# Kernel tuning notes

Hardware: AMD Instinct MI355X
Metric: run time of the kernel (lower is better)

## Reference

```python
import jax, jax.numpy as jnp
import numpy as np

B, C, H, W = 32, 512, 32, 32
R = C // 2  # reduced channels for key/prod projections


def setup_inputs() -> dict:
    key = jax.random.key(0)
    ks = jax.random.split(key, 8)
    s_in = 1.0 / np.sqrt(C)
    return {
        "x": jax.random.normal(ks[0], (B, C, H, W), jnp.float32),
        "Wk": jax.random.normal(ks[1], (R, C), jnp.float32) * s_in,
        "bk": jax.random.normal(ks[2], (R,), jnp.float32) * s_in,
        "Wp": jax.random.normal(ks[3], (R, C), jnp.float32) * s_in,
        "bp": jax.random.normal(ks[4], (R,), jnp.float32) * s_in,
        "Wv": jax.random.normal(ks[5], (C, C), jnp.float32) * s_in,
        "bv": jax.random.normal(ks[6], (C,), jnp.float32) * s_in,
        "param": jax.random.normal(ks[7], (1,), jnp.float32),
    }


def _conv1x1(x, Wmat, b):
    # 1x1 conv on NCHW == per-pixel channel matmul
    return jnp.einsum('bchw,oc->bohw', x, Wmat) + b[None, :, None, None]


def reference(x, Wk, bk, Wp, bp, Wv, bv, param):
    b, c, h, w = x.shape
    hw = h * w
    f_key = _conv1x1(x, Wk, bk).reshape(b, -1, hw).transpose(0, 2, 1)  # [B,HW,R]
    f_prod = _conv1x1(x, Wp, bp).reshape(b, -1, hw)                    # [B,R,HW]
    f_value = _conv1x1(x, Wv, bv).reshape(b, -1, hw)                   # [B,C,HW]
    energy = jnp.einsum('bnr,brm->bnm', f_key, f_prod)                 # [B,HW,HW]
    similarity = jax.nn.softmax(energy, axis=-1)
    # bmm(f_value, similarity^T): out[b,c,n] = sum_m f_value[b,c,m] * sim[b,n,m]
    attended = jnp.einsum('bcm,bnm->bcn', f_value, similarity).reshape(b, c, h, w)
    return x + attended * param
```

## Files before the change

### kernel.cpp

```cpp
#include <hip/hip_runtime.h>
#include <hip/hip_bf16.h>

#define BATCH 32
#define CCH   512
#define HWSZ  1024
#define RCH   256

typedef __attribute__((ext_vector_type(8))) _Float16 f16x8;
typedef __attribute__((ext_vector_type(4))) float f32x4;

__device__ __forceinline__ ushort f2h(float f) {
    _Float16 h = (_Float16)f;
    ushort u; __builtin_memcpy(&u, &h, 2);
    return u;
}
__device__ __forceinline__ float h2f(ushort u) {
    _Float16 h; __builtin_memcpy(&h, &u, 2);
    return (float)h;
}

__device__ __forceinline__ void load_lds16(const void* g, void* l) {
    __builtin_amdgcn_global_load_lds((const __attribute__((address_space(1))) void*)g,
                                     (__attribute__((address_space(3))) void*)l,
                                     16, 0, 0);
}

__device__ __forceinline__ void xcd_swizzle(int& bx, int& by, int& bz) {
    int gx = gridDim.x, gy = gridDim.y;
    int n   = gx * gy * gridDim.z;
    int lin = bx + gx * (by + gy * bz);
    int cpx = n >> 3;
    int s = (lin & 7) * cpx + (lin >> 3);
    bx = s % gx; s /= gx;
    by = s % gy;
    bz = s / gy;
}

__global__ __launch_bounds__(256) void k_pre(
    const float* __restrict__ x, ushort* __restrict__ xt,
    const float* __restrict__ Wk, const float* __restrict__ bk,
    const float* __restrict__ Wp, const float* __restrict__ bp,
    const float* __restrict__ Wv,
    ushort* __restrict__ Wkp_h, ushort* __restrict__ Wv_h, float* __restrict__ bias_kp)
{
    __shared__ float tile[64][68];
    int t = threadIdx.x;
    if (blockIdx.z == 32) {
        int base = ((blockIdx.y * 16 + blockIdx.x) * 256 + t) * 8;
        int o = base >> 9, c = base & 511;
        const float* srcKP = (o < 256) ? (Wk + (size_t)o * 512 + c)
                                       : (Wp + (size_t)(o - 256) * 512 + c);
        float4 a0 = *(const float4*)srcKP;
        float4 a1 = *(const float4*)(srcKP + 4);
        ushort4 h0, h1;
        h0.x = f2h(a0.x); h0.y = f2h(a0.y); h0.z = f2h(a0.z); h0.w = f2h(a0.w);
        h1.x = f2h(a1.x); h1.y = f2h(a1.y); h1.z = f2h(a1.z); h1.w = f2h(a1.w);
        *(ushort4*)&Wkp_h[base] = h0;
        *(ushort4*)&Wkp_h[base + 4] = h1;
        float4 v0 = *(const float4*)(Wv + base);
        float4 v1 = *(const float4*)(Wv + base + 4);
        h0.x = f2h(v0.x); h0.y = f2h(v0.y); h0.z = f2h(v0.z); h0.w = f2h(v0.w);
        h1.x = f2h(v1.x); h1.y = f2h(v1.y); h1.z = f2h(v1.z); h1.w = f2h(v1.w);
        *(ushort4*)&Wv_h[base] = h0;
        *(ushort4*)&Wv_h[base + 4] = h1;
        if (c == 0) bias_kp[o] = (o < 256) ? bk[o] : bp[o - 256];
        return;
    }
    int b  = blockIdx.z;
    int c0 = blockIdx.y * 64;
    int n0 = blockIdx.x * 64;
    const float* xb = x + (size_t)b * CCH * HWSZ;
    int tc  = t >> 4;
    int tn4 = (t & 15) * 4;
    #pragma unroll
    for (int i = 0; i < 4; ++i) {
        int c = tc + i * 16;
        *(float4*)&tile[c][tn4] = *(const float4*)&xb[(size_t)(c0 + c) * HWSZ + n0 + tn4];
    }
    __syncthreads();
    ushort* oh = xt + (size_t)b * HWSZ * CCH;
    int tn  = t >> 4;
    int tc4 = (t & 15) * 4;
    #pragma unroll
    for (int i = 0; i < 4; ++i) {
        int n = tn + i * 16;
        ushort4 h;
        h.x = f2h(tile[tc4 + 0][n]);
        h.y = f2h(tile[tc4 + 1][n]);
        h.z = f2h(tile[tc4 + 2][n]);
        h.w = f2h(tile[tc4 + 3][n]);
        *(ushort4*)&oh[(size_t)(n0 + n) * CCH + c0 + tc4] = h;
    }
}

template<int MODE>
__global__ __launch_bounds__(512, 4) void k_gemm8(
    const ushort* __restrict__ A, const ushort* __restrict__ B,
    int lda, int ldb, long aBatch, long bBatch,
    float* __restrict__ outF, ushort* __restrict__ out16,
    long oBatch, int ldo,
    const float* __restrict__ bias,
    const float* __restrict__ xres, const float* __restrict__ param,
    int NT)
{
    __shared__ ushort lds[2][12288];
    int bx = blockIdx.x, by = blockIdx.y, bz = blockIdx.z;
    xcd_swizzle(bx, by, bz);
    const int z  = bz;
    const int m0 = bx * 128;
    const int n0 = by * 256;
    const int t    = threadIdx.x;
    const int lane = t & 63;
    const int w    = t >> 6;
    const int wm = w >> 2, wn = w & 3;
    const int l15 = lane & 15;
    const int hi  = lane >> 4;
    const int G   = hi ^ ((lane >> 1) & 3);

    const ushort* Ab = A + (size_t)z * aBatch;
    const ushort* Bb = B + (size_t)z * bBatch;

    const int sr = t >> 2;
    const int sg = (t & 3) ^ ((t >> 3) & 3);

    f32x4 acc[4][4] = {};
    f16x8 a[4], b01[2], b23[2];

#define STAGE(slot, kt) do {                                                 \
        size_t sa_ = (size_t)(m0 + sr) * lda + (kt) * 32 + sg * 8;           \
        load_lds16(Ab + sa_, &lds[slot][t * 8]);                             \
        size_t sb_ = (size_t)(n0 + sr) * ldb + (kt) * 32 + sg * 8;           \
        load_lds16(Bb + sb_, &lds[slot][4096 + t * 8]);                      \
        load_lds16(Bb + sb_ + (size_t)128 * ldb, &lds[slot][8192 + t * 8]);  \
    } while (0)

#define RD_ALL(slot) do {                                                    \
        _Pragma("unroll")                                                    \
        for (int ni = 0; ni < 2; ++ni)                                       \
            b01[ni] = *(const f16x8*)&lds[slot][4096 + (wn * 64 + ni * 16 + l15) * 32 + G * 8]; \
        _Pragma("unroll")                                                    \
        for (int ni = 0; ni < 2; ++ni)                                       \
            b23[ni] = *(const f16x8*)&lds[slot][4096 + (wn * 64 + 32 + ni * 16 + l15) * 32 + G * 8]; \
        _Pragma("unroll")                                                    \
        for (int mi = 0; mi < 4; ++mi)                                       \
            a[mi] = *(const f16x8*)&lds[slot][(wm * 64 + mi * 16 + l15) * 32 + G * 8]; \
    } while (0)

#define BAR() __builtin_amdgcn_s_barrier()
#define WLG(N) do { asm volatile("s_waitcnt lgkmcnt(" #N ")" ::: "memory");  \
                    __builtin_amdgcn_sched_barrier(0); } while (0)
#define WVM(N) asm volatile("s_waitcnt vmcnt(" #N ")" ::: "memory")

#define MM4(mi) do {                                                         \
        acc[mi][0] = __builtin_amdgcn_mfma_f32_16x16x32_f16(a[mi], b01[0], acc[mi][0], 0, 0, 0); \
        acc[mi][1] = __builtin_amdgcn_mfma_f32_16x16x32_f16(a[mi], b01[1], acc[mi][1], 0, 0, 0); \
        acc[mi][2] = __builtin_amdgcn_mfma_f32_16x16x32_f16(a[mi], b23[0], acc[mi][2], 0, 0, 0); \
        acc[mi][3] = __builtin_amdgcn_mfma_f32_16x16x32_f16(a[mi], b23[1], acc[mi][3], 0, 0, 0); \
    } while (0)

#define MFMA_PIPE() do {                                                     \
        WLG(3); MM4(0); WLG(2); MM4(1); WLG(1); MM4(2); WLG(0); MM4(3);      \
    } while (0)

    STAGE(0, 0);
    WVM(0);
    BAR();

    for (int j = 0; j < NT - 1; ++j) {
        int cur = j & 1;
        STAGE(cur ^ 1, j + 1);
        RD_ALL(cur);
        MFMA_PIPE();
        WVM(0);
        BAR();
    }
    {
        RD_ALL(1);
        MFMA_PIPE();
    }

    if (MODE == 3) {
        float* fbuf = (float*)lds;
        const float prm = param[0];
        float*       ob = outF + (size_t)z * oBatch;
        const float* xb = xres + (size_t)z * oBatch;
        #pragma unroll
        for (int h = 0; h < 4; ++h) {
            asm volatile("s_waitcnt lgkmcnt(0)" ::: "memory");
            BAR();
            if (wn == h) {
                #pragma unroll
                for (int mi = 0; mi < 4; ++mi)
                    #pragma unroll
                    for (int ni = 0; ni < 4; ++ni) {
                        int cc = (ni >> 1) * 32 + (ni & 1) * 16 + l15;
                        int nn = (wm * 64 + mi * 16 + hi * 4) ^ ((cc & 7) << 2);
                        *(f32x4*)&fbuf[cc * 128 + nn] = acc[mi][ni];
                    }
            }
            asm volatile("s_waitcnt lgkmcnt(0)" ::: "memory");
            BAR();
            #pragma unroll
            for (int rr = 0; rr < 4; ++rr) {
                int cc  = w * 8 + rr * 2 + (lane >> 5);
                int col = (lane & 31) * 4;
                f32x4 o4 = *(const f32x4*)&fbuf[cc * 128 + (col ^ ((cc & 7) << 2))];
                size_t g = (size_t)(n0 + h * 64 + cc) * ldo + m0 + col;
                float4 xv = *(const float4*)&xb[g];
                float4 ov;
                ov.x = xv.x + o4[0] * prm;
                ov.y = xv.y + o4[1] * prm;
                ov.z = xv.z + o4[2] * prm;
                ov.w = xv.w + o4[3] * prm;
                *(float4*)&ob[g] = ov;
            }
        }
    } else {
        #pragma unroll
        for (int mi = 0; mi < 4; ++mi) {
            #pragma unroll
            for (int ni = 0; ni < 4; ++ni) {
                int gc  = n0 + wn * 64 + (ni >> 1) * 32 + (ni & 1) * 16 + l15;
                int gr0 = m0 + wm * 64 + mi * 16 + hi * 4;
                #pragma unroll
                for (int jj = 0; jj < 4; ++jj) {
                    int gr = gr0 + jj;
                    float v = acc[mi][ni][jj];
                    if (MODE == 0) {
                        v += bias[gc];
                        out16[(size_t)gr * ldo + gc] = f2h(v);
                    } else if (MODE == 1) {
                        v += bias[gr];
                        out16[(size_t)z * oBatch + (size_t)gr * ldo + gc] = f2h(v);
                    } else {
                        out16[(size_t)z * oBatch + (size_t)gr * ldo + gc] = f2h(v);
                    }
                }
            }
        }
    }
#undef STAGE
#undef RD_ALL
#undef BAR
#undef WLG
#undef WVM
#undef MM4
#undef MFMA_PIPE
}

__global__ __launch_bounds__(256) void k_softmax(ushort* __restrict__ E)
{
    int t    = threadIdx.x;
    int rowi = t >> 7;
    int tl   = t & 127;
    ushort* row = E + (size_t)(blockIdx.x * 2 + rowi) * HWSZ;
    uint4 u = *(const uint4*)&row[tl * 8];
    float v[8];
    v[0] = h2f(u.x & 0xffff); v[1] = h2f(u.x >> 16);
    v[2] = h2f(u.y & 0xffff); v[3] = h2f(u.y >> 16);
    v[4] = h2f(u.z & 0xffff); v[5] = h2f(u.z >> 16);
    v[6] = h2f(u.w & 0xffff); v[7] = h2f(u.w >> 16);
    float mx = v[0];
    #pragma unroll
    for (int i = 1; i < 8; ++i) mx = fmaxf(mx, v[i]);
    #pragma unroll
    for (int off = 1; off < 64; off <<= 1)
        mx = fmaxf(mx, __shfl_xor(mx, off));
    __shared__ float redm[2][2];
    __shared__ float reds[2][2];
    int lane = t & 63, wv = (t >> 6) & 1;
    if (lane == 0) redm[rowi][wv] = mx;
    __syncthreads();
    mx = fmaxf(redm[rowi][0], redm[rowi][1]);
    float s = 0.f;
    #pragma unroll
    for (int i = 0; i < 8; ++i) { v[i] = __expf(v[i] - mx); s += v[i]; }
    #pragma unroll
    for (int off = 1; off < 64; off <<= 1)
        s += __shfl_xor(s, off);
    if (lane == 0) reds[rowi][wv] = s;
    __syncthreads();
    s = reds[rowi][0] + reds[rowi][1];
    float inv = 1.0f / s;
    uint4 o;
    o.x = (unsigned)f2h(v[0] * inv) | ((unsigned)f2h(v[1] * inv) << 16);
    o.y = (unsigned)f2h(v[2] * inv) | ((unsigned)f2h(v[3] * inv) << 16);
    o.z = (unsigned)f2h(v[4] * inv) | ((unsigned)f2h(v[5] * inv) << 16);
    o.w = (unsigned)f2h(v[6] * inv) | ((unsigned)f2h(v[7] * inv) << 16);
    *(uint4*)&row[tl * 8] = o;
}

extern "C" void kernel_launch(void* const* d_in, const int* in_sizes, int n_in,
                              void* d_out, int out_size, void* d_ws, size_t ws_size,
                              hipStream_t stream)
{
    const float* x    = (const float*)d_in[0];
    const float* Wk   = (const float*)d_in[1];
    const float* bk   = (const float*)d_in[2];
    const float* Wp   = (const float*)d_in[3];
    const float* bp   = (const float*)d_in[4];
    const float* Wv   = (const float*)d_in[5];
    const float* bv   = (const float*)d_in[6];
    const float* prm  = (const float*)d_in[7];
    float* out = (float*)d_out;
    char* ws = (char*)d_ws;

    const size_t SZ16 = (size_t)BATCH * HWSZ * CCH * 2;
    ushort* xt    = (ushort*)(ws + 0);
    ushort* KPt   = (ushort*)(ws + SZ16);
    ushort* fv    = (ushort*)(ws + 2 * SZ16);
    ushort* E     = (ushort*)(ws + 3 * SZ16);
    char* wbase   = ws + 3 * SZ16 + (size_t)BATCH * HWSZ * HWSZ * 2;
    ushort* Wkp_h = (ushort*)(wbase);
    ushort* Wv_h  = (ushort*)(wbase + 524288);
    float*  bias_kp = (float*)(wbase + 2 * 524288);

    k_pre<<<dim3(16, 8, 33), 256, 0, stream>>>(
        x, xt, Wk, bk, Wp, bp, Wv, Wkp_h, Wv_h, bias_kp);

    k_gemm8<0><<<dim3(256, 2, 1), 512, 0, stream>>>(
        xt, Wkp_h, CCH, CCH, 0, 0,
        nullptr, KPt, 0, CCH,
        bias_kp, nullptr, nullptr, CCH / 32);

    k_gemm8<1><<<dim3(4, 4, 32), 512, 0, stream>>>(
        Wv_h, xt, CCH, CCH, 0, (long)HWSZ * CCH,
        nullptr, fv, (long)CCH * HWSZ, HWSZ,
        bv, nullptr, nullptr, CCH / 32);

    k_gemm8<2><<<dim3(8, 4, 32), 512, 0, stream>>>(
        KPt, KPt + RCH, CCH, CCH,
        (long)HWSZ * CCH, (long)HWSZ * CCH,
        nullptr, E, (long)HWSZ * HWSZ, HWSZ,
        nullptr, nullptr, nullptr, RCH / 32);

    k_softmax<<<BATCH * HWSZ / 2, 256, 0, stream>>>(E);

    k_gemm8<3><<<dim3(8, 2, 32), 512, 0, stream>>>(
        E, fv, HWSZ, HWSZ,
        (long)HWSZ * HWSZ, (long)CCH * HWSZ,
        out, nullptr, (long)CCH * HWSZ, HWSZ,
        nullptr, x, prm, HWSZ / 32);
}
```

Before: 179.2 us.

## Fuse energy GEMM, softmax and value GEMM into flash-attention kernel

Replaces the separate energy GEMM, row softmax and attention-value GEMM with one flash-attention style kernel that uses an online softmax. Each block handles 128 queries for one batch, streams 64-key tiles of the prod projection and value into LDS, and rescales its accumulators. This removes the round trip of the 32x1024x1024 fp16 energy matrix through global memory and two kernel launches. In exchange there are only 256 blocks with one block per CU, a single-buffered tile load with a full wait each iteration, and the 128x512 accumulator per block puts heavy pressure on registers.

```diff
diff --git a/kernel.cpp b/kernel.cpp
--- a/kernel.cpp
+++ b/kernel.cpp
@@ -14,15 +14,15 @@
     ushort u; __builtin_memcpy(&u, &h, 2);
     return u;
 }
-__device__ __forceinline__ float h2f(ushort u) {
-    _Float16 h; __builtin_memcpy(&h, &u, 2);
-    return (float)h;
-}
 
 __device__ __forceinline__ void load_lds16(const void* g, void* l) {
     __builtin_amdgcn_global_load_lds((const __attribute__((address_space(1))) void*)g,
                                      (__attribute__((address_space(3))) void*)l,
                                      16, 0, 0);
+}
+
+__device__ __forceinline__ f32x4 mfma16(f16x8 a, f16x8 b, f32x4 c) {
+    return __builtin_amdgcn_mfma_f32_16x16x32_f16(a, b, c, 0, 0, 0);
 }
 
 __device__ __forceinline__ void xcd_swizzle(int& bx, int& by, int& bz) {
@@ -97,11 +97,8 @@
 __global__ __launch_bounds__(512, 4) void k_gemm8(
     const ushort* __restrict__ A, const ushort* __restrict__ B,
     int lda, int ldb, long aBatch, long bBatch,
-    float* __restrict__ outF, ushort* __restrict__ out16,
-    long oBatch, int ldo,
-    const float* __restrict__ bias,
-    const float* __restrict__ xres, const float* __restrict__ param,
-    int NT)
+    ushort* __restrict__ out16, long oBatch, int ldo,
+    const float* __restrict__ bias, int NT)
 {
     __shared__ ushort lds[2][12288];
     int bx = blockIdx.x, by = blockIdx.y, bz = blockIdx.z;
@@ -152,10 +149,10 @@
 #define WVM(N) asm volatile("s_waitcnt vmcnt(" #N ")" ::: "memory")
 
 #define MM4(mi) do {                                                         \
-        acc[mi][0] = __builtin_amdgcn_mfma_f32_16x16x32_f16(a[mi], b01[0], acc[mi][0], 0, 0, 0); \
-        acc[mi][1] = __builtin_amdgcn_mfma_f32_16x16x32_f16(a[mi], b01[1], acc[mi][1], 0, 0, 0); \
-        acc[mi][2] = __builtin_amdgcn_mfma_f32_16x16x32_f16(a[mi], b23[0], acc[mi][2], 0, 0, 0); \
-        acc[mi][3] = __builtin_amdgcn_mfma_f32_16x16x32_f16(a[mi], b23[1], acc[mi][3], 0, 0, 0); \
+        acc[mi][0] = mfma16(a[mi], b01[0], acc[mi][0]);                      \
+        acc[mi][1] = mfma16(a[mi], b01[1], acc[mi][1]);                      \
+        acc[mi][2] = mfma16(a[mi], b23[0], acc[mi][2]);                      \
+        acc[mi][3] = mfma16(a[mi], b23[1], acc[mi][3]);                      \
     } while (0)
 
 #define MFMA_PIPE() do {                                                     \
@@ -165,7 +162,6 @@
     STAGE(0, 0);
     WVM(0);
     BAR();
-
     for (int j = 0; j < NT - 1; ++j) {
         int cur = j & 1;
         STAGE(cur ^ 1, j + 1);
@@ -174,67 +170,25 @@
         WVM(0);
         BAR();
     }
-    {
-        RD_ALL(1);
-        MFMA_PIPE();
-    }
-
-    if (MODE == 3) {
-        float* fbuf = (float*)lds;
-        const float prm = param[0];
-        float*       ob = outF + (size_t)z * oBatch;
-        const float* xb = xres + (size_t)z * oBatch;
-        #pragma unroll
-        for (int h = 0; h < 4; ++h) {
-            asm volatile("s_waitcnt lgkmcnt(0)" ::: "memory");
-            BAR();
-            if (wn == h) {
-                #pragma unroll
-                for (int mi = 0; mi < 4; ++mi)
-                    #pragma unroll
-                    for (int ni = 0; ni < 4; ++ni) {
-                        int cc = (ni >> 1) * 32 + (ni & 1) * 16 + l15;
-                        int nn = (wm * 64 + mi * 16 + hi * 4) ^ ((cc & 7) << 2);
-                        *(f32x4*)&fbuf[cc * 128 + nn] = acc[mi][ni];
-                    }
-            }
-            asm volatile("s_waitcnt lgkmcnt(0)" ::: "memory");
-            BAR();
-            #pragma unroll
-            for (int rr = 0; rr < 4; ++rr) {
-                int cc  = w * 8 + rr * 2 + (lane >> 5);
-                int col = (lane & 31) * 4;
-                f32x4 o4 = *(const f32x4*)&fbuf[cc * 128 + (col ^ ((cc & 7) << 2))];
-                size_t g = (size_t)(n0 + h * 64 + cc) * ldo + m0 + col;
-                float4 xv = *(const float4*)&xb[g];
-                float4 ov;
-                ov.x = xv.x + o4[0] * prm;
-                ov.y = xv.y + o4[1] * prm;
-                ov.z = xv.z + o4[2] * prm;
-                ov.w = xv.w + o4[3] * prm;
-                *(float4*)&ob[g] = ov;
-            }
-        }
-    } else {
-        #pragma unroll
-        for (int mi = 0; mi < 4; ++mi) {
-            #pragma unroll
-            for (int ni = 0; ni < 4; ++ni) {
-                int gc  = n0 + wn * 64 + (ni >> 1) * 32 + (ni & 1) * 16 + l15;
-                int gr0 = m0 + wm * 64 + mi * 16 + hi * 4;
-                #pragma unroll
-                for (int jj = 0; jj < 4; ++jj) {
-                    int gr = gr0 + jj;
-                    float v = acc[mi][ni][jj];
-                    if (MODE == 0) {
-                        v += bias[gc];
-                        out16[(size_t)gr * ldo + gc] = f2h(v);
-                    } else if (MODE == 1) {
-                        v += bias[gr];
-                        out16[(size_t)z * oBatch + (size_t)gr * ldo + gc] = f2h(v);
-                    } else {
-                        out16[(size_t)z * oBatch + (size_t)gr * ldo + gc] = f2h(v);
-                    }
+    RD_ALL(1);
+    MFMA_PIPE();
+
+    #pragma unroll
+    for (int mi = 0; mi < 4; ++mi) {
+        #pragma unroll
+        for (int ni = 0; ni < 4; ++ni) {
+            int gc  = n0 + wn * 64 + (ni >> 1) * 32 + (ni & 1) * 16 + l15;
+            int gr0 = m0 + wm * 64 + mi * 16 + hi * 4;
+            #pragma unroll
+            for (int jj = 0; jj < 4; ++jj) {
+                int gr = gr0 + jj;
+                float v = acc[mi][ni][jj];
+                if (MODE == 0) {
+                    v += bias[gc];
+                    out16[(size_t)gr * ldo + gc] = f2h(v);
+                } else {
+                    v += bias[gr];
+                    out16[(size_t)z * oBatch + (size_t)gr * ldo + gc] = f2h(v);
                 }
             }
         }
@@ -248,46 +202,208 @@
 #undef MFMA_PIPE
 }
 
-__global__ __launch_bounds__(256) void k_softmax(ushort* __restrict__ E)
+__global__ __launch_bounds__(512, 1) void k_attn(
+    const ushort* __restrict__ KPt, const ushort* __restrict__ fv,
+    const float* __restrict__ x, float* __restrict__ out,
+    const float* __restrict__ param)
 {
-    int t    = threadIdx.x;
-    int rowi = t >> 7;
-    int tl   = t & 127;
-    ushort* row = E + (size_t)(blockIdx.x * 2 + rowi) * HWSZ;
-    uint4 u = *(const uint4*)&row[tl * 8];
-    float v[8];
-    v[0] = h2f(u.x & 0xffff); v[1] = h2f(u.x >> 16);
-    v[2] = h2f(u.y & 0xffff); v[3] = h2f(u.y >> 16);
-    v[4] = h2f(u.z & 0xffff); v[5] = h2f(u.z >> 16);
-    v[6] = h2f(u.w & 0xffff); v[7] = h2f(u.w >> 16);
-    float mx = v[0];
+    __shared__ char smem[116224];
+    ushort* PT = (ushort*)smem;
+    ushort* FV = (ushort*)(smem + 32768);
+    ushort* PP = (ushort*)(smem + 98304);
+    float*  SC = (float*)(smem + 114688);
+    float*  IL = (float*)(smem + 115200);
+    float*  fbuf = (float*)smem;
+
+    int bx = blockIdx.x, by = blockIdx.y, bz = blockIdx.z;
+    xcd_swizzle(bx, by, bz);
+    const int z = by, q0 = bx * 128;
+    const int t = threadIdx.x, lane = t & 63, w = t >> 6;
+    const int l15 = lane & 15, hi = lane >> 4;
+    const int wq = w >> 2, wc = w & 3;
+
+    const ushort* KPb = KPt + (size_t)z * HWSZ * CCH;
+    const ushort* fvb = fv + (size_t)z * CCH * HWSZ;
+
+    f16x8 qf[8];
+    {
+        const ushort* qrow = KPb + (size_t)(q0 + w * 16 + l15) * CCH + hi * 8;
+        #pragma unroll
+        for (int ks = 0; ks < 8; ++ks)
+            qf[ks] = *(const f16x8*)(qrow + ks * 32);
+    }
+
+#define STAGE_TILE(kv0) do {                                                 \
+        _Pragma("unroll")                                                    \
+        for (int i = 0; i < 4; ++i) {                                        \
+            int s_ = i * 512 + t; int kvl = s_ >> 5; int g_ = s_ & 31;       \
+            size_t src = (size_t)((kv0) + kvl) * CCH + RCH + (size_t)((g_ ^ (kvl & 7)) * 8); \
+            load_lds16(KPb + src, PT + s_ * 8);                              \
+        }                                                                    \
+        _Pragma("unroll")                                                    \
+        for (int i = 0; i < 8; ++i) {                                        \
+            int s_ = i * 512 + t; int cl = s_ >> 3; int g_ = s_ & 7;         \
+            size_t src = (size_t)cl * HWSZ + (kv0) + (size_t)((g_ ^ (cl & 7)) * 8); \
+            load_lds16(fvb + src, FV + s_ * 8);                              \
+        }                                                                    \
+    } while (0)
+
+    f32x4 acc[4][8] = {};
+    float mj[4] = {-3e38f, -3e38f, -3e38f, -3e38f};
+    float lj[4] = {0.f, 0.f, 0.f, 0.f};
+    const int rbase = w * 16 + hi * 4;
+
+    STAGE_TILE(0);
+    asm volatile("s_waitcnt vmcnt(0)" ::: "memory");
+    __builtin_amdgcn_s_barrier();
+
+    for (int tl = 0; tl < 16; ++tl) {
+        f32x4 sacc[4] = {};
+        #pragma unroll
+        for (int n = 0; n < 4; ++n) {
+            int kv = n * 16 + l15;
+            #pragma unroll
+            for (int kh = 0; kh < 2; ++kh) {
+                f16x8 pb[4];
+                #pragma unroll
+                for (int ks = 0; ks < 4; ++ks) {
+                    int G = (kh * 4 + ks) * 4 + hi;
+                    pb[ks] = *(const f16x8*)(PT + kv * 256 + (G ^ (kv & 7)) * 8);
+                }
+                #pragma unroll
+                for (int ks = 0; ks < 4; ++ks)
+                    sacc[n] = mfma16(qf[kh * 4 + ks], pb[ks], sacc[n]);
+            }
+        }
+        f32x4 scv;
+        #pragma unroll
+        for (int j = 0; j < 4; ++j) {
+            float mx = fmaxf(fmaxf(sacc[0][j], sacc[1][j]), fmaxf(sacc[2][j], sacc[3][j]));
+            mx = fmaxf(mx, __shfl_xor(mx, 1));
+            mx = fmaxf(mx, __shfl_xor(mx, 2));
+            mx = fmaxf(mx, __shfl_xor(mx, 4));
+            mx = fmaxf(mx, __shfl_xor(mx, 8));
+            float mn = fmaxf(mj[j], mx);
+            float sc = __expf(mj[j] - mn);
+            float s = 0.f;
+            #pragma unroll
+            for (int n = 0; n < 4; ++n) {
+                float p = __expf(sacc[n][j] - mn);
+                sacc[n][j] = p; s += p;
+            }
+            s += __shfl_xor(s, 1);
+            s += __shfl_xor(s, 2);
+            s += __shfl_xor(s, 4);
+            s += __shfl_xor(s, 8);
+            lj[j] = lj[j] * sc + s;
+            mj[j] = mn;
+            scv[j] = sc;
+        }
+        #pragma unroll
+        for (int n = 0; n < 4; ++n) {
+            int col = n * 16 + l15;
+            #pragma unroll
+            for (int j = 0; j < 4; ++j) {
+                int row = rbase + j;
+                PP[row * 64 + ((col >> 3) ^ (row & 7)) * 8 + (col & 7)] = f2h(sacc[n][j]);
+            }
+        }
+        if (l15 == 0) *(f32x4*)&SC[rbase] = scv;
+        __syncthreads();
+
+        #pragma unroll
+        for (int mi = 0; mi < 4; ++mi) {
+            f32x4 sv = *(const f32x4*)&SC[wq * 64 + mi * 16 + hi * 4];
+            #pragma unroll
+            for (int ci = 0; ci < 8; ++ci)
+                #pragma unroll
+                for (int j = 0; j < 4; ++j)
+                    acc[mi][ci][j] *= sv[j];
+        }
+        #pragma unroll
+        for (int ks = 0; ks < 2; ++ks) {
+            f16x8 am[4];
+            #pragma unroll
+            for (int mi = 0; mi < 4; ++mi) {
+                int q = wq * 64 + mi * 16 + l15;
+                int G = ks * 4 + hi;
+                am[mi] = *(const f16x8*)(PP + q * 64 + (G ^ (q & 7)) * 8);
+            }
+            #pragma unroll
+            for (int ch = 0; ch < 2; ++ch) {
+                f16x8 bf_[4];
+                #pragma unroll
+                for (int c4 = 0; c4 < 4; ++c4) {
+                    int ci = ch * 4 + c4;
+                    int c = wc * 128 + ci * 16 + l15;
+                    int G = ks * 4 + hi;
+                    bf_[c4] = *(const f16x8*)(FV + c * 64 + (G ^ (c & 7)) * 8);
+                }
+                #pragma unroll
+                for (int mi = 0; mi < 4; ++mi)
+                    #pragma unroll
+                    for (int c4 = 0; c4 < 4; ++c4)
+                        acc[mi][ch * 4 + c4] = mfma16(am[mi], bf_[c4], acc[mi][ch * 4 + c4]);
+            }
+        }
+        __syncthreads();
+        if (tl < 15) {
+            STAGE_TILE((tl + 1) * 64);
+            asm volatile("s_waitcnt vmcnt(0)" ::: "memory");
+            __builtin_amdgcn_s_barrier();
+        }
+    }
+
+    if (l15 == 0) {
+        f32x4 iv;
+        #pragma unroll
+        for (int j = 0; j < 4; ++j) iv[j] = 1.0f / lj[j];
+        *(f32x4*)&IL[rbase] = iv;
+    }
+    __syncthreads();
+    const float prm = param[0];
+    float*       ob = out + (size_t)z * CCH * HWSZ;
+    const float* xb = x + (size_t)z * CCH * HWSZ;
+    f32x4 il4[4];
     #pragma unroll
-    for (int i = 1; i < 8; ++i) mx = fmaxf(mx, v[i]);
+    for (int mi = 0; mi < 4; ++mi)
+        il4[mi] = *(const f32x4*)&IL[wq * 64 + mi * 16 + hi * 4];
+
     #pragma unroll
-    for (int off = 1; off < 64; off <<= 1)
-        mx = fmaxf(mx, __shfl_xor(mx, off));
-    __shared__ float redm[2][2];
-    __shared__ float reds[2][2];
-    int lane = t & 63, wv = (t >> 6) & 1;
-    if (lane == 0) redm[rowi][wv] = mx;
-    __syncthreads();
-    mx = fmaxf(redm[rowi][0], redm[rowi][1]);
-    float s = 0.f;
-    #pragma unroll
-    for (int i = 0; i < 8; ++i) { v[i] = __expf(v[i] - mx); s += v[i]; }
-    #pragma unroll
-    for (int off = 1; off < 64; off <<= 1)
-        s += __shfl_xor(s, off);
-    if (lane == 0) reds[rowi][wv] = s;
-    __syncthreads();
-    s = reds[rowi][0] + reds[rowi][1];
-    float inv = 1.0f / s;
-    uint4 o;
-    o.x = (unsigned)f2h(v[0] * inv) | ((unsigned)f2h(v[1] * inv) << 16);
-    o.y = (unsigned)f2h(v[2] * inv) | ((unsigned)f2h(v[3] * inv) << 16);
-    o.z = (unsigned)f2h(v[4] * inv) | ((unsigned)f2h(v[5] * inv) << 16);
-    o.w = (unsigned)f2h(v[6] * inv) | ((unsigned)f2h(v[7] * inv) << 16);
-    *(uint4*)&row[tl * 8] = o;
+    for (int h = 0; h < 8; ++h) {
+        __syncthreads();
+        if (wc == (h >> 1)) {
+            #pragma unroll
+            for (int mi = 0; mi < 4; ++mi)
+                #pragma unroll
+                for (int c4 = 0; c4 < 4; ++c4) {
+                    int ci = (h & 1) * 4 + c4;
+                    int cc = c4 * 16 + l15;
+                    int nn = wq * 64 + mi * 16 + hi * 4;
+                    f32x4 v;
+                    #pragma unroll
+                    for (int j = 0; j < 4; ++j)
+                        v[j] = acc[mi][ci][j] * il4[mi][j] * prm;
+                    *(f32x4*)&fbuf[cc * 128 + (nn ^ ((cc & 7) << 2))] = v;
+                }
+        }
+        __syncthreads();
+        #pragma unroll
+        for (int rr = 0; rr < 4; ++rr) {
+            int cc  = w * 8 + rr * 2 + (lane >> 5);
+            int col = (lane & 31) * 4;
+            f32x4 o4 = *(const f32x4*)&fbuf[cc * 128 + (col ^ ((cc & 7) << 2))];
+            size_t g = (size_t)(h * 64 + cc) * HWSZ + q0 + col;
+            float4 xv = *(const float4*)&xb[g];
+            float4 ov;
+            ov.x = xv.x + o4[0];
+            ov.y = xv.y + o4[1];
+            ov.z = xv.z + o4[2];
+            ov.w = xv.w + o4[3];
+            *(float4*)&ob[g] = ov;
+        }
+    }
+#undef STAGE_TILE
 }
 
 extern "C" void kernel_launch(void* const* d_in, const int* in_sizes, int n_in,
@@ -309,8 +425,7 @@
     ushort* xt    = (ushort*)(ws + 0);
     ushort* KPt   = (ushort*)(ws + SZ16);
     ushort* fv    = (ushort*)(ws + 2 * SZ16);
-    ushort* E     = (ushort*)(ws + 3 * SZ16);
-    char* wbase   = ws + 3 * SZ16 + (size_t)BATCH * HWSZ * HWSZ * 2;
+    char* wbase   = ws + 3 * SZ16;
     ushort* Wkp_h = (ushort*)(wbase);
     ushort* Wv_h  = (ushort*)(wbase + 524288);
     float*  bias_kp = (float*)(wbase + 2 * 524288);
@@ -320,25 +435,11 @@
 
     k_gemm8<0><<<dim3(256, 2, 1), 512, 0, stream>>>(
         xt, Wkp_h, CCH, CCH, 0, 0,
-        nullptr, KPt, 0, CCH,
-        bias_kp, nullptr, nullptr, CCH / 32);
+        KPt, 0, CCH, bias_kp, CCH / 32);
 
     k_gemm8<1><<<dim3(4, 4, 32), 512, 0, stream>>>(
         Wv_h, xt, CCH, CCH, 0, (long)HWSZ * CCH,
-        nullptr, fv, (long)CCH * HWSZ, HWSZ,
-        bv, nullptr, nullptr, CCH / 32);
-
-    k_gemm8<2><<<dim3(8, 4, 32), 512, 0, stream>>>(
-        KPt, KPt + RCH, CCH, CCH,
-        (long)HWSZ * CCH, (long)HWSZ * CCH,
-        nullptr, E, (long)HWSZ * HWSZ, HWSZ,
-        nullptr, nullptr, nullptr, RCH / 32);
-
-    k_softmax<<<BATCH * HWSZ / 2, 256, 0, stream>>>(E);
-
-    k_gemm8<3><<<dim3(8, 2, 32), 512, 0, stream>>>(
-        E, fv, HWSZ, HWSZ,
-        (long)HWSZ * HWSZ, (long)CCH * HWSZ,
-        out, nullptr, (long)CCH * HWSZ, HWSZ,
-        nullptr, x, prm, HWSZ / 32);
-}
+        fv, (long)CCH * HWSZ, HWSZ, bv, CCH / 32);
+
+    k_attn<<<dim3(8, 32, 1), 512, 0, stream>>>(KPt, fv, x, out, prm);
+}
```

After: 289.1 us. 61.3% more time.
